# Optimization experiments

Hardware: AMD Instinct MI355X
Metric: run time of the kernel (lower is better)

Reference implementation:

```python
import jax, jax.numpy as jnp
import numpy as np

DIM = 384
H = 65536
P = 3
CORR = 2 * 49 * P * P  # 882


def _lin(x, W, b):
    # x: [H, Cin], W: [Cout, Cin], b: [Cout] -> [H, Cout] (1x1 conv == linear over channels)
    return x @ W.T + b


def setup_inputs() -> dict:
    key = jax.random.key(0)
    ks = jax.random.split(key, 20)
    f32 = jnp.float32

    def rn(k, shape, s=0.02):
        return jax.random.normal(k, shape, f32) * s

    return {
        "net": jax.random.normal(ks[0], (1, DIM, H, 1), f32),
        "inp": jax.random.normal(ks[1], (1, DIM, H, 1), f32),
        "corr": jax.random.normal(ks[2], (1, CORR, H, 1), f32),
        "ii": jax.random.normal(ks[3], (1, 1, H, 1), f32),
        "jj": jax.random.normal(ks[4], (1, 1, H, 1), f32),
        "kk": jax.random.normal(ks[5], (1, 1, H, 1), f32),
        # keep_conv: Conv2d(1,1,1,bias=False) with weight zeroed (frozen)
        "kw": jnp.zeros((), f32),
        # corr_conv: Linear(882->384), ReLU, Linear(384->384), ReLU, Linear(384->384)
        "cc_w1": rn(ks[6], (DIM, CORR)), "cc_b1": jnp.zeros((DIM,), f32),
        "cc_w2": rn(ks[7], (DIM, DIM)), "cc_b2": jnp.zeros((DIM,), f32),
        "cc_w3": rn(ks[8], (DIM, DIM)), "cc_b3": jnp.zeros((DIM,), f32),
        # c1 / c2: Linear(384->384), ReLU, Linear(384->384)
        "c1_w1": rn(ks[9], (DIM, DIM)), "c1_b1": jnp.zeros((DIM,), f32),
        "c1_w2": rn(ks[10], (DIM, DIM)), "c1_b2": jnp.zeros((DIM,), f32),
        "c2_w1": rn(ks[11], (DIM, DIM)), "c2_b1": jnp.zeros((DIM,), f32),
        "c2_w2": rn(ks[12], (DIM, DIM)), "c2_b2": jnp.zeros((DIM,), f32),
        # heads: Linear(384->2)
        "d_w": rn(ks[13], (2, DIM)), "d_b": jnp.zeros((2,), f32),
        "w_w": rn(ks[14], (2, DIM)), "w_b": jnp.zeros((2,), f32),
    }


def reference(net, inp, corr, ii, jj, kk, kw,
              cc_w1, cc_b1, cc_w2, cc_b2, cc_w3, cc_b3,
              c1_w1, c1_b1, c1_w2, c1_b2,
              c2_w1, c2_b1, c2_w2, c2_b2,
              d_w, d_b, w_w, w_b):
    # [1,C,H,1] -> [H,C]
    x = net[0, :, :, 0].T
    y = inp[0, :, :, 0].T
    c = corr[0, :, :, 0].T

    # dummy keep_conv path (zero weight, further scaled by 0.0)
    dummy = (ii + jj + kk)[0, 0, :, 0] * kw  # [H]
    x = x + dummy[:, None] * 0.0

    # corr_conv
    cc = _lin(jax.nn.relu(_lin(jax.nn.relu(_lin(c, cc_w1, cc_b1)), cc_w2, cc_b2)), cc_w3, cc_b3)
    x = x + y + cc

    # net = net + c1(net) + c2(net), both branches read the same pre-update net
    b1 = _lin(jax.nn.relu(_lin(x, c1_w1, c1_b1)), c1_w2, c1_b2)
    b2 = _lin(jax.nn.relu(_lin(x, c2_w1, c2_b1)), c2_w2, c2_b2)
    x = x + b1 + b2

    r = jax.nn.relu(x)
    d_out = _lin(r, d_w, d_b)                      # [H,2]
    w_out = jax.nn.sigmoid(_lin(r, w_w, w_b))      # [H,2]

    # back to [1,C,H,1]
    net_out = x.T[None, :, :, None]
    d_out = d_out.T[None, :, :, None]
    w_out = w_out.T[None, :, :, None]
    return (net_out, d_out, w_out)
```

## Files before the change

### kernel.cpp

```cpp
#include <hip/hip_runtime.h>
#include <hip/hip_bf16.h>

#define H 65536
#define DIMC 384

typedef __bf16 bf16x8 __attribute__((ext_vector_type(8)));
typedef float f32x4 __attribute__((ext_vector_type(4)));

__device__ __forceinline__ unsigned short f2bf(float x) {
    return __builtin_bit_cast(unsigned short, __float2bfloat16(x));
}
__device__ __forceinline__ float bf2f(unsigned short u) {
    return __bfloat162float(__builtin_bit_cast(__hip_bfloat16, u));
}

__global__ __launch_bounds__(256) void wconv_k(
    const float* __restrict__ w1, const float* __restrict__ w2, const float* __restrict__ w3,
    const float* __restrict__ c11, const float* __restrict__ c12,
    const float* __restrict__ c21, const float* __restrict__ c22,
    unsigned short* __restrict__ dst)
{
    int m = blockIdx.y;
    const float* src; unsigned short* d; int K, Kp;
    if (m == 0) { src = w1; d = dst; K = 882; Kp = 896; }
    else {
        switch (m) {
            case 1: src = w2;  break;
            case 2: src = w3;  break;
            case 3: src = c11; break;
            case 4: src = c12; break;
            case 5: src = c21; break;
            default: src = c22; break;
        }
        K = 384; Kp = 384;
        d = dst + 344064 + (m - 1) * 147456;
    }
    int gid = blockIdx.x * 256 + threadIdx.x;
    if (gid < 384 * Kp) {
        int n = gid / Kp;
        int k = gid - n * Kp;
        d[gid] = f2bf(k < K ? src[n * K + k] : 0.f);
    }
}

__global__ __launch_bounds__(256) void corr_tconv(const float* __restrict__ src,
                                                  unsigned short* __restrict__ dst)
{
    __shared__ float tile[64][65];
    int hb = blockIdx.x * 64;
    int kb = blockIdx.y * 64;
    int t = threadIdx.x;
    int col = t & 63, r4 = t >> 6;
    #pragma unroll
    for (int p = 0; p < 16; ++p) {
        int row = p * 4 + r4;
        int k = kb + row;
        tile[row][col] = (k < 882) ? src[(size_t)k * H + hb + col] : 0.f;
    }
    __syncthreads();
    #pragma unroll
    for (int p = 0; p < 16; ++p) {
        int hrow = p * 4 + r4;
        dst[(size_t)(hb + hrow) * 896 + kb + col] = f2bf(tile[col][hrow]);
    }
}

template<int MODE>
__global__ __launch_bounds__(256) void gemm_k(
    const unsigned short* __restrict__ W,
    const unsigned short* __restrict__ A,
    const float* __restrict__ bias,
    const float* __restrict__ aux0,
    const float* __restrict__ aux1,
    const unsigned short* __restrict__ auxb,
    unsigned short* __restrict__ outb,
    float* __restrict__ outf,
    int Kp)
{
    __shared__ unsigned short Wt[128 * 64];
    __shared__ unsigned short At[128 * 64];
    const int tid  = threadIdx.x;
    const int lane = tid & 63;
    const int wave = tid >> 6;
    const int quad = lane >> 4;
    const int l15  = lane & 15;
    const int h0 = blockIdx.x * 128;
    const int c0 = blockIdx.y * 128;
    const int cw = (wave & 1) * 64;
    const int hw = (wave >> 1) * 64;

    const unsigned short* Wbase = W + (size_t)c0 * Kp;
    const unsigned short* Abase = A + (size_t)h0 * Kp;

    f32x4 acc[4][4];
    #pragma unroll
    for (int i = 0; i < 4; ++i)
        #pragma unroll
        for (int j = 0; j < 4; ++j)
            acc[i][j] = f32x4{0.f, 0.f, 0.f, 0.f};

    const int srow = tid >> 3;
    const int skc  = (tid & 7) * 8;

    for (int kt = 0; kt < Kp; kt += 64) {
        __syncthreads();
        #pragma unroll
        for (int i = 0; i < 4; ++i) {
            const unsigned short* g = Wbase + (size_t)(i * 32 + srow) * Kp + kt + skc;
            char* lb = (char*)Wt + (i * 256 + wave * 64) * 16;
            __builtin_amdgcn_global_load_lds((__attribute__((address_space(1))) void*)(void*)g,
                                             (__attribute__((address_space(3))) void*)lb, 16, 0, 0);
        }
        #pragma unroll
        for (int i = 0; i < 4; ++i) {
            const unsigned short* g = Abase + (size_t)(i * 32 + srow) * Kp + kt + skc;
            char* lb = (char*)At + (i * 256 + wave * 64) * 16;
            __builtin_amdgcn_global_load_lds((__attribute__((address_space(1))) void*)(void*)g,
                                             (__attribute__((address_space(3))) void*)lb, 16, 0, 0);
        }
        __syncthreads();

        const uint4* Wv = (const uint4*)Wt;
        const uint4* Av = (const uint4*)At;
        #pragma unroll
        for (int ks = 0; ks < 2; ++ks) {
            uint4 aw[4], bx[4];
            #pragma unroll
            for (int ci = 0; ci < 4; ++ci) aw[ci] = Wv[(cw + ci * 16 + l15) * 8 + ks * 4 + quad];
            #pragma unroll
            for (int hi = 0; hi < 4; ++hi) bx[hi] = Av[(hw + hi * 16 + l15) * 8 + ks * 4 + quad];
            #pragma unroll
            for (int ci = 0; ci < 4; ++ci)
                #pragma unroll
                for (int hi = 0; hi < 4; ++hi)
                    acc[ci][hi] = __builtin_amdgcn_mfma_f32_16x16x32_bf16(
                        __builtin_bit_cast(bf16x8, aw[ci]),
                        __builtin_bit_cast(bf16x8, bx[hi]),
                        acc[ci][hi], 0, 0, 0);
        }
    }

    #pragma unroll
    for (int ci = 0; ci < 4; ++ci) {
        const int c = c0 + cw + ci * 16 + quad * 4;
        f32x4 b4 = *(const f32x4*)(bias + c);
        #pragma unroll
        for (int hi = 0; hi < 4; ++hi) {
            const int h = h0 + hw + hi * 16 + l15;
            const size_t base = (size_t)h * DIMC + c;
            f32x4 v = acc[ci][hi] + b4;
            if constexpr (MODE == 1) {
                #pragma unroll
                for (int r = 0; r < 4; ++r)
                    v[r] += aux0[(size_t)(c + r) * H + h] + aux1[(size_t)(c + r) * H + h];
            }
            if constexpr (MODE == 3) {
                v += *(const f32x4*)(aux0 + base);
                ushort4 u = *(const ushort4*)(auxb + base);
                v[0] += bf2f(u.x); v[1] += bf2f(u.y);
                v[2] += bf2f(u.z); v[3] += bf2f(u.w);
            }
            if constexpr (MODE == 1) {
                *(f32x4*)(outf + base) = v;
            }
            if constexpr (MODE == 3) {
                #pragma unroll
                for (int r = 0; r < 4; ++r)
                    outf[(size_t)(c + r) * H + h] = v[r];
            }
            f32x4 s = v;
            if constexpr (MODE == 0 || MODE == 3) {
                s[0] = fmaxf(s[0], 0.f); s[1] = fmaxf(s[1], 0.f);
                s[2] = fmaxf(s[2], 0.f); s[3] = fmaxf(s[3], 0.f);
            }
            ushort4 o;
            o.x = f2bf(s[0]); o.y = f2bf(s[1]); o.z = f2bf(s[2]); o.w = f2bf(s[3]);
            *(ushort4*)(outb + base) = o;
        }
    }
}

__global__ __launch_bounds__(256) void heads_k(
    const unsigned short* __restrict__ r,
    const float* __restrict__ dW, const float* __restrict__ dB,
    const float* __restrict__ wW, const float* __restrict__ wB,
    float* __restrict__ out)
{
    __shared__ float wl[1536];
    int tid = threadIdx.x;
    for (int i = tid; i < 1536; i += 256)
        wl[i] = (i < 768) ? dW[i] : wW[i - 768];
    __syncthreads();
    int wave = tid >> 6, lane = tid & 63;
    int h = blockIdx.x * 4 + wave;
    const unsigned short* rp = r + (size_t)h * 384 + lane * 6;
    int c = lane * 6;
    float s0 = 0.f, s1 = 0.f, s2 = 0.f, s3 = 0.f;
    #pragma unroll
    for (int i = 0; i < 6; ++i) {
        float rv = bf2f(rp[i]);
        s0 += rv * wl[c + i];
        s1 += rv * wl[384 + c + i];
        s2 += rv * wl[768 + c + i];
        s3 += rv * wl[1152 + c + i];
    }
    #pragma unroll
    for (int m = 32; m >= 1; m >>= 1) {
        s0 += __shfl_xor(s0, m, 64);
        s1 += __shfl_xor(s1, m, 64);
        s2 += __shfl_xor(s2, m, 64);
        s3 += __shfl_xor(s3, m, 64);
    }
    if (lane == 0) {
        float* od = out + (size_t)384 * H;
        float* ow = out + (size_t)386 * H;
        od[h]     = s0 + dB[0];
        od[H + h] = s1 + dB[1];
        ow[h]     = 1.f / (1.f + __expf(-(s2 + wB[0])));
        ow[H + h] = 1.f / (1.f + __expf(-(s3 + wB[1])));
    }
}

extern "C" void kernel_launch(void* const* d_in, const int* in_sizes, int n_in,
                              void* d_out, int out_size, void* d_ws, size_t ws_size,
                              hipStream_t stream)
{
    const float* net   = (const float*)d_in[0];
    const float* inp   = (const float*)d_in[1];
    const float* corr  = (const float*)d_in[2];
    const float* cc_w1 = (const float*)d_in[7];
    const float* cc_b1 = (const float*)d_in[8];
    const float* cc_w2 = (const float*)d_in[9];
    const float* cc_b2 = (const float*)d_in[10];
    const float* cc_w3 = (const float*)d_in[11];
    const float* cc_b3 = (const float*)d_in[12];
    const float* c1_w1 = (const float*)d_in[13];
    const float* c1_b1 = (const float*)d_in[14];
    const float* c1_w2 = (const float*)d_in[15];
    const float* c1_b2 = (const float*)d_in[16];
    const float* c2_w1 = (const float*)d_in[17];
    const float* c2_b1 = (const float*)d_in[18];
    const float* c2_w2 = (const float*)d_in[19];
    const float* c2_b2 = (const float*)d_in[20];
    const float* d_wp  = (const float*)d_in[21];
    const float* d_bp  = (const float*)d_in[22];
    const float* w_wp  = (const float*)d_in[23];
    const float* w_bp  = (const float*)d_in[24];
    float* out = (float*)d_out;

    char* ws = (char*)d_ws;
    size_t off = 0;
    auto carve = [&](size_t bytes) -> char* {
        char* p = ws + off;
        off += (bytes + 255) & ~(size_t)255;
        return p;
    };
    unsigned short* Wreg  = (unsigned short*)carve((size_t)1228800 * 2);
    unsigned short* corrb = (unsigned short*)carve((size_t)H * 896 * 2);
    unsigned short* t1    = (unsigned short*)carve((size_t)H * 384 * 2);
    unsigned short* t2    = (unsigned short*)carve((size_t)H * 384 * 2);
    float*          xf    = (float*)carve((size_t)H * 384 * 4);
    unsigned short* xb    = (unsigned short*)carve((size_t)H * 384 * 2);

    unsigned short* w1b  = Wreg;
    unsigned short* w2b  = Wreg + 344064;
    unsigned short* w3b  = w2b + 147456;
    unsigned short* c11b = w3b + 147456;
    unsigned short* c12b = c11b + 147456;
    unsigned short* c21b = c12b + 147456;
    unsigned short* c22b = c21b + 147456;

    wconv_k<<<dim3(1344, 7), 256, 0, stream>>>(cc_w1, cc_w2, cc_w3, c1_w1, c1_w2, c2_w1, c2_w2, Wreg);
    corr_tconv<<<dim3(1024, 14), 256, 0, stream>>>(corr, corrb);

    gemm_k<0><<<dim3(512, 3), 256, 0, stream>>>(w1b, corrb, cc_b1, nullptr, nullptr, nullptr, t1, nullptr, 896);
    gemm_k<0><<<dim3(512, 3), 256, 0, stream>>>(w2b, t1, cc_b2, nullptr, nullptr, nullptr, t2, nullptr, 384);
    gemm_k<1><<<dim3(512, 3), 256, 0, stream>>>(w3b, t2, cc_b3, net, inp, nullptr, xb, xf, 384);
    gemm_k<0><<<dim3(512, 3), 256, 0, stream>>>(c11b, xb, c1_b1, nullptr, nullptr, nullptr, t1, nullptr, 384);
    gemm_k<2><<<dim3(512, 3), 256, 0, stream>>>(c12b, t1, c1_b2, nullptr, nullptr, nullptr, t2, nullptr, 384);
    gemm_k<0><<<dim3(512, 3), 256, 0, stream>>>(c21b, xb, c2_b1, nullptr, nullptr, nullptr, corrb, nullptr, 384);
    gemm_k<3><<<dim3(512, 3), 256, 0, stream>>>(c22b, corrb, c2_b2, xf, nullptr, t2, t1, out, 384);

    heads_k<<<H / 4, 256, 0, stream>>>(t1, d_wp, d_bp, w_wp, w_bp, out);
}
```

Before: 1.015 ms.

## Concatenate c1/c2 branch weights into two wider GEMMs

The two residual branches read the same input, so their first-layer weights are stacked into one 768-wide output GEMM. Their second-layer weights are concatenated along K into one 768-deep GEMM, which sums both branch outputs inside the accumulator. This cuts four GEMM launches to two and removes the bf16 intermediate round trip of branch 1's output, along with the extra reread of xb. Biases are pre-summed in the weight conversion kernel. Branch 1's output is no longer rounded to bf16 before the sum, which slightly changes numerics.

```diff
diff --git a/kernel.cpp b/kernel.cpp
--- a/kernel.cpp
+++ b/kernel.cpp
@@ -16,31 +16,41 @@
 
 __global__ __launch_bounds__(256) void wconv_k(
     const float* __restrict__ w1, const float* __restrict__ w2, const float* __restrict__ w3,
-    const float* __restrict__ c11, const float* __restrict__ c12,
-    const float* __restrict__ c21, const float* __restrict__ c22,
-    unsigned short* __restrict__ dst)
+    const float* __restrict__ c11, const float* __restrict__ c21,
+    const float* __restrict__ c12, const float* __restrict__ c22,
+    const float* __restrict__ b11, const float* __restrict__ b21,
+    const float* __restrict__ b12, const float* __restrict__ b22,
+    unsigned short* __restrict__ dst, float* __restrict__ biasf)
 {
     int m = blockIdx.y;
-    const float* src; unsigned short* d; int K, Kp;
-    if (m == 0) { src = w1; d = dst; K = 882; Kp = 896; }
-    else {
-        switch (m) {
-            case 1: src = w2;  break;
-            case 2: src = w3;  break;
-            case 3: src = c11; break;
-            case 4: src = c12; break;
-            case 5: src = c21; break;
-            default: src = c22; break;
-        }
-        K = 384; Kp = 384;
-        d = dst + 344064 + (m - 1) * 147456;
-    }
     int gid = blockIdx.x * 256 + threadIdx.x;
-    if (gid < 384 * Kp) {
-        int n = gid / Kp;
-        int k = gid - n * Kp;
-        d[gid] = f2bf(k < K ? src[n * K + k] : 0.f);
-    }
+    if (m == 7) {
+        if (gid < 384)       biasf[gid] = b11[gid];
+        else if (gid < 768)  biasf[gid] = b21[gid - 384];
+        else if (gid < 1152) biasf[gid] = b12[gid - 768] + b22[gid - 768];
+        return;
+    }
+    if (m == 0) {
+        if (gid < 344064) {
+            int n = gid / 896, k = gid - n * 896;
+            dst[gid] = f2bf(k < 882 ? w1[n * 882 + k] : 0.f);
+        }
+        return;
+    }
+    if (gid >= 147456) return;
+    const float* src; size_t doff; int Kp = 384, koff = 0;
+    switch (m) {
+        case 1:  src = c12; doff = 933888; Kp = 768; break;
+        default: src = nullptr; doff = 0; break;
+    }
+    if (m == 1)      { src = w2;  doff = 344064;          Kp = 384; koff = 0;   }
+    else if (m == 2) { src = w3;  doff = 491520;          Kp = 384; koff = 0;   }
+    else if (m == 3) { src = c11; doff = 638976;          Kp = 384; koff = 0;   }
+    else if (m == 4) { src = c21; doff = 638976 + 147456; Kp = 384; koff = 0;   }
+    else if (m == 5) { src = c12; doff = 933888;          Kp = 768; koff = 0;   }
+    else             { src = c22; doff = 933888;          Kp = 768; koff = 384; }
+    int n = gid / 384, k = gid - n * 384;
+    dst[doff + (size_t)n * Kp + koff + k] = f2bf(src[gid]);
 }
 
 __global__ __launch_bounds__(256) void corr_tconv(const float* __restrict__ src,
@@ -72,10 +82,9 @@
     const float* __restrict__ bias,
     const float* __restrict__ aux0,
     const float* __restrict__ aux1,
-    const unsigned short* __restrict__ auxb,
     unsigned short* __restrict__ outb,
     float* __restrict__ outf,
-    int Kp)
+    int Kp, int ldo)
 {
     __shared__ unsigned short Wt[128 * 64];
     __shared__ unsigned short At[128 * 64];
@@ -147,23 +156,16 @@
         #pragma unroll
         for (int hi = 0; hi < 4; ++hi) {
             const int h = h0 + hw + hi * 16 + l15;
-            const size_t base = (size_t)h * DIMC + c;
+            const size_t base = (size_t)h * ldo + c;
             f32x4 v = acc[ci][hi] + b4;
             if constexpr (MODE == 1) {
                 #pragma unroll
                 for (int r = 0; r < 4; ++r)
                     v[r] += aux0[(size_t)(c + r) * H + h] + aux1[(size_t)(c + r) * H + h];
+                *(f32x4*)(outf + base) = v;
             }
             if constexpr (MODE == 3) {
                 v += *(const f32x4*)(aux0 + base);
-                ushort4 u = *(const ushort4*)(auxb + base);
-                v[0] += bf2f(u.x); v[1] += bf2f(u.y);
-                v[2] += bf2f(u.z); v[3] += bf2f(u.w);
-            }
-            if constexpr (MODE == 1) {
-                *(f32x4*)(outf + base) = v;
-            }
-            if constexpr (MODE == 3) {
                 #pragma unroll
                 for (int r = 0; r < 4; ++r)
                     outf[(size_t)(c + r) * H + h] = v[r];
@@ -261,25 +263,23 @@
     unsigned short* t2    = (unsigned short*)carve((size_t)H * 384 * 2);
     float*          xf    = (float*)carve((size_t)H * 384 * 4);
     unsigned short* xb    = (unsigned short*)carve((size_t)H * 384 * 2);
-
-    unsigned short* w1b  = Wreg;
-    unsigned short* w2b  = Wreg + 344064;
-    unsigned short* w3b  = w2b + 147456;
-    unsigned short* c11b = w3b + 147456;
-    unsigned short* c12b = c11b + 147456;
-    unsigned short* c21b = c12b + 147456;
-    unsigned short* c22b = c21b + 147456;
-
-    wconv_k<<<dim3(1344, 7), 256, 0, stream>>>(cc_w1, cc_w2, cc_w3, c1_w1, c1_w2, c2_w1, c2_w2, Wreg);
+    float*          biasf = (float*)carve((size_t)1152 * 4);
+
+    unsigned short* w1b = Wreg;
+    unsigned short* w2b = Wreg + 344064;
+    unsigned short* w3b = Wreg + 491520;
+    unsigned short* cAb = Wreg + 638976;
+    unsigned short* cBb = Wreg + 933888;
+
+    wconv_k<<<dim3(1344, 8), 256, 0, stream>>>(cc_w1, cc_w2, cc_w3, c1_w1, c2_w1, c1_w2, c2_w2,
+                                               c1_b1, c2_b1, c1_b2, c2_b2, Wreg, biasf);
     corr_tconv<<<dim3(1024, 14), 256, 0, stream>>>(corr, corrb);
 
-    gemm_k<0><<<dim3(512, 3), 256, 0, stream>>>(w1b, corrb, cc_b1, nullptr, nullptr, nullptr, t1, nullptr, 896);
-    gemm_k<0><<<dim3(512, 3), 256, 0, stream>>>(w2b, t1, cc_b2, nullptr, nullptr, nullptr, t2, nullptr, 384);
-    gemm_k<1><<<dim3(512, 3), 256, 0, stream>>>(w3b, t2, cc_b3, net, inp, nullptr, xb, xf, 384);
-    gemm_k<0><<<dim3(512, 3), 256, 0, stream>>>(c11b, xb, c1_b1, nullptr, nullptr, nullptr, t1, nullptr, 384);
-    gemm_k<2><<<dim3(512, 3), 256, 0, stream>>>(c12b, t1, c1_b2, nullptr, nullptr, nullptr, t2, nullptr, 384);
-    gemm_k<0><<<dim3(512, 3), 256, 0, stream>>>(c21b, xb, c2_b1, nullptr, nullptr, nullptr, corrb, nullptr, 384);
-    gemm_k<3><<<dim3(512, 3), 256, 0, stream>>>(c22b, corrb, c2_b2, xf, nullptr, t2, t1, out, 384);
+    gemm_k<0><<<dim3(512, 3), 256, 0, stream>>>(w1b, corrb, cc_b1, nullptr, nullptr, t1, nullptr, 896, 384);
+    gemm_k<0><<<dim3(512, 3), 256, 0, stream>>>(w2b, t1, cc_b2, nullptr, nullptr, t2, nullptr, 384, 384);
+    gemm_k<1><<<dim3(512, 3), 256, 0, stream>>>(w3b, t2, cc_b3, net, inp, xb, xf, 384, 384);
+    gemm_k<0><<<dim3(512, 6), 256, 0, stream>>>(cAb, xb, biasf, nullptr, nullptr, corrb, nullptr, 384, 768);
+    gemm_k<3><<<dim3(512, 3), 256, 0, stream>>>(cBb, corrb, biasf + 768, xf, nullptr, t1, out, 768, 384);
 
     heads_k<<<H / 4, 256, 0, stream>>>(t1, d_wp, d_bp, w_wp, w_bp, out);
 }
```

New measurement: 977.6 us. 1.04x faster.
